# Performance work log

Measured on AMD Instinct MI355X. Metric: run time of the kernel, lower is better.

## Reference

```python
import jax, jax.numpy as jnp
import numpy as np

B, H, W, C = 16, 112, 112, 128
WS, SS, NH = 7, 3, 4  # window_size, shift_size, num_heads
EPS = 1e-5


def _ln(x, g, b):
    m = jnp.mean(x, axis=-1, keepdims=True)
    v = jnp.var(x, axis=-1, keepdims=True)
    return (x - m) * jax.lax.rsqrt(v + EPS) * g + b


def _rel_index(w):
    # standard Swin relative-position index, [w*w, w*w] int
    coords = np.stack(np.meshgrid(np.arange(w), np.arange(w), indexing='ij'))  # [2,w,w]
    flat = coords.reshape(2, -1)                      # [2, N]
    rel = (flat[:, :, None] - flat[:, None, :]).transpose(1, 2, 0)  # [N,N,2]
    rel = rel + (w - 1)
    return rel[..., 0] * (2 * w - 1) + rel[..., 1]


def _attn_mask(Hp, Wp, w, s):
    # standard Swin shifted-window attention mask, [nW, N, N] float32 (0 / -100)
    img = np.zeros((Hp, Wp))
    cnt = 0
    for hs in (slice(0, -w), slice(-w, -s), slice(-s, None)):
        for ws_ in (slice(0, -w), slice(-w, -s), slice(-s, None)):
            img[hs, ws_] = cnt
            cnt += 1
    mw = img.reshape(Hp // w, w, Wp // w, w).transpose(0, 2, 1, 3).reshape(-1, w * w)
    d = mw[:, None, :] - mw[:, :, None]
    return np.where(d != 0, -100.0, 0.0).astype(np.float32)


def setup_inputs() -> dict:
    key = jax.random.key(0)
    ks = jax.random.split(key, 8)
    f = lambda k, shape: jax.random.normal(k, shape, dtype=jnp.float32) * 0.02
    return dict(
        x=jax.random.normal(ks[0], (B, H, W, C), dtype=jnp.float32),
        norm1_g=jnp.ones((C,), jnp.float32), norm1_b=jnp.zeros((C,), jnp.float32),
        qkv_w=f(ks[1], (C, 3 * C)), qkv_b=jnp.zeros((3 * C,), jnp.float32),
        rel_table=f(ks[2], ((2 * WS - 1) ** 2, NH)),
        proj_w=f(ks[3], (C, C)), proj_b=jnp.zeros((C,), jnp.float32),
        norm2_g=jnp.ones((C,), jnp.float32), norm2_b=jnp.zeros((C,), jnp.float32),
        fc1_w=f(ks[4], (C, 4 * C)), fc1_b=jnp.zeros((4 * C,), jnp.float32),
        fc2_w=f(ks[5], (4 * C, C)), fc2_b=jnp.zeros((C,), jnp.float32),
    )


def reference(x, norm1_g, norm1_b, qkv_w, qkv_b, rel_table, proj_w, proj_b,
              norm2_g, norm2_b, fc1_w, fc1_b, fc2_w, fc2_b):
    w, s, nH = WS, SS, NH
    hd = C // nH
    N = w * w
    scale = hd ** -0.5

    shortcut = x
    xn = _ln(x, norm1_g, norm1_b)
    # cyclic shift (H, W already multiples of w -> no padding)
    xs = jnp.roll(xn, (-s, -s), axis=(1, 2)) if s > 0 else xn
    # window partition -> [B*nW, N, C]
    wins = xs.reshape(B, H // w, w, W // w, w, C).transpose(0, 1, 3, 2, 4, 5).reshape(-1, N, C)

    qkv = wins @ qkv_w + qkv_b  # [M, N, 3C]
    q, k, v = [t.reshape(-1, N, nH, hd).transpose(0, 2, 1, 3)
               for t in jnp.split(qkv, 3, axis=-1)]
    attn = jnp.einsum('mhqd,mhkd->mhqk', q * scale, k)  # [M, nH, N, N]

    idx = _rel_index(w)  # static numpy [N, N]
    bias = rel_table[idx.reshape(-1)].reshape(N, N, nH).transpose(2, 0, 1)  # [nH, N, N]
    attn = attn + bias[None]

    if s > 0:
        mask = jnp.asarray(_attn_mask(H, W, w, s))  # [nW, N, N] static
        nW = mask.shape[0]
        attn = (attn.reshape(B, nW, nH, N, N) + mask[None, :, None]).reshape(-1, nH, N, N)

    attn = jax.nn.softmax(attn, axis=-1)
    out = jnp.einsum('mhqk,mhkd->mhqd', attn, v).transpose(0, 2, 1, 3).reshape(-1, N, C)
    out = out @ proj_w + proj_b

    # window reverse + unshift
    x_attn = out.reshape(B, H // w, W // w, w, w, C).transpose(0, 1, 3, 2, 4, 5).reshape(B, H, W, C)
    if s > 0:
        x_attn = jnp.roll(x_attn, (s, s), axis=(1, 2))

    x1 = shortcut + x_attn
    xn2 = _ln(x1, norm2_g, norm2_b)
    hdd = jax.nn.gelu(xn2 @ fc1_w + fc1_b, approximate=False)  # torch nn.GELU (exact)
    return x1 + (hdd @ fc2_w + fc2_b)
```

## Files before the change

kernel.cpp:

```cpp
#include <hip/hip_runtime.h>
#include <stdint.h>

typedef unsigned short u16;
typedef unsigned int   u32;
typedef __attribute__((ext_vector_type(8))) short bh8;
typedef __attribute__((ext_vector_type(4))) float f32x4;

#define SCALE 0.17677669529663687f
#define MFMA  __builtin_amdgcn_mfma_f32_16x16x32_bf16

#define WS_QKV  0
#define WS_PROJ 49152
#define WS_F1   65536
#define WS_F2   131072
#define WS_M    196608
#define WS_QB   327680
#define WS_S1   328448
#define WS_T1   329472

__device__ __forceinline__ u16 f2bf(float f){
    u32 i; __builtin_memcpy(&i,&f,4); i += 0x7fffu + ((i>>16)&1u); return (u16)(i>>16);
}
__device__ __forceinline__ u32 cvtpk(float lo, float hi){
    u32 r; asm("v_cvt_pk_bf16_f32 %0, %1, %2" : "=v"(r) : "v"(lo), "v"(hi)); return r;
}
__device__ __forceinline__ float rcpf(float v){
    float r; asm("v_rcp_f32 %0, %1" : "=v"(r) : "v"(v)); return r;
}
__device__ __forceinline__ float gelu_f(float x){
    float ax = fabsf(x);
    float z  = ax * 0.70710678118654752f;
    float t  = rcpf(fmaf(0.3275911f, z, 1.0f));
    float p  = t * fmaf(t, fmaf(t, fmaf(t, fmaf(t, 1.061405429f, -1.453152027f),
                                        1.421413741f), -0.284496736f), 0.254829592f);
    float e  = __expf(-z * z);
    float y  = fmaf(-p, e, 1.0f);
    return fmaf(0.5f * ax, y, 0.5f * x);
}
union BH8U { bh8 v; u32 u[4]; };

__global__ void prep_k(const float* __restrict__ qkvw, const float* __restrict__ projw,
                       const float* __restrict__ f1w,  const float* __restrict__ f2w,
                       const float* __restrict__ rel,  const float* __restrict__ qkvb,
                       const float* __restrict__ n2g,  const float* __restrict__ n2b,
                       const float* __restrict__ f1b,  u16* __restrict__ ws)
{
    int idx = blockIdx.x * 256 + threadIdx.x;
    if (idx < 49152) {
        int c = idx / 384, j = idx % 384;
        float v = qkvw[idx] * (j < 128 ? SCALE : 1.0f);
        ws[WS_QKV + j * 128 + c] = f2bf(v);
    } else if (idx < 65536) {
        int i = idx - 49152; int k = i >> 7, j = i & 127;
        int pk = (k & ~31) | ((k & 15) << 1) | ((k >> 4) & 1);
        ws[WS_PROJ + j * 128 + pk] = f2bf(projw[i]);
    } else if (idx < 131072) {
        int i = idx - 65536; int c = i >> 9, j = i & 511;
        ws[WS_F1 + j * 128 + c] = f2bf(f1w[i] * n2g[c]);
    } else if (idx < 196608) {
        int i = idx - 131072; int k = i >> 7, j = i & 127;
        ws[WS_F2 + j * 512 + k] = f2bf(f2w[i]);
    } else if (idx < 262144) {
        int m = idx - 196608;
        int jr = m & 3, lane = (m >> 2) & 63, tct = (m >> 8) & 15;
        int h = (m >> 12) & 3, cls = (m >> 14) & 3;
        int rt = tct >> 2, ct = tct & 3;
        int row = rt * 16 + (lane >> 4) * 4 + jr, key = ct * 16 + (lane & 15);
        float v;
        if (row < 49 && key < 49) {
            int ri = row / 7, rc = row % 7, ki = key / 7, kc = key % 7;
            v = rel[((ri - ki + 6) * 13 + (rc - kc + 6)) * 4 + h];
            int rH = (cls & 2) ? (ri < 4 ? 1 : 2) : 0, rW = (cls & 1) ? (rc < 4 ? 1 : 2) : 0;
            int kH = (cls & 2) ? (ki < 4 ? 1 : 2) : 0, kW = (cls & 1) ? (kc < 4 ? 1 : 2) : 0;
            if (rH * 3 + rW != kH * 3 + kW) v -= 100.0f;
        } else v = -30000.0f;
        ((float*)(ws + WS_M))[m] = v;
    } else if (idx < 262528) {
        int j = idx - 262144;
        ((float*)(ws + WS_QB))[j] = qkvb[j] * (j < 128 ? SCALE : 1.0f);
    } else if (idx < 263040) {
        int j = idx - 262528;
        float s1 = 0.f, t1 = 0.f;
        for (int c = 0; c < 128; ++c) {
            float w = f1w[c * 512 + j];
            s1 = fmaf(n2g[c], w, s1);
            t1 = fmaf(n2b[c], w, t1);
        }
        ((float*)(ws + WS_S1))[j] = s1;
        ((float*)(ws + WS_T1))[j] = f1b[j] + t1;
    }
}

__global__ __launch_bounds__(256, 3) void swin_attn_k(
    const float* __restrict__ x, const float* __restrict__ n1g, const float* __restrict__ n1b,
    const float* __restrict__ projb, const u16* __restrict__ ws, float* __restrict__ out)
{
    __shared__ u16 arena[16384];
    __shared__ u16 vt[9216];
    const int tid = threadIdx.x, h = tid >> 6, lane = tid & 63;
    const int c15 = lane & 15, g = lane >> 4;
    const int m = blockIdx.x, b = m >> 8, hb = (m >> 4) & 15, wb = m & 15;
    const int cls = ((hb == 15) ? 2 : 0) | ((wb == 15) ? 1 : 0);
    const float* QB = (const float*)(ws + WS_QB);
    const float* Mb = (const float*)(ws + WS_M) + (size_t)((cls * 4 + h) * 16) * 256;

    {
        const int t = h * 16 + (lane >> 2), ss = lane & 3;
        if (t < 49) {
            const int td = (t * 37) >> 8, tm = t - td * 7;
            int hs = hb * 7 + td + 3;  if (hs >= 112) hs -= 112;
            int wsw = wb * 7 + tm + 3; if (wsw >= 112) wsw -= 112;
            const float* px = x + (size_t)((b * 112 + hs) * 112 + wsw) * 128 + ss * 32;
            float4 xv[8];
            #pragma unroll
            for (int i = 0; i < 8; ++i) xv[i] = *(const float4*)(px + i * 4);
            float s = 0.f, q = 0.f;
            #pragma unroll
            for (int i = 0; i < 8; ++i) {
                s += xv[i].x + xv[i].y + xv[i].z + xv[i].w;
                q += xv[i].x*xv[i].x + xv[i].y*xv[i].y + xv[i].z*xv[i].z + xv[i].w*xv[i].w;
            }
            s += __shfl_xor(s, 1); q += __shfl_xor(q, 1);
            s += __shfl_xor(s, 2); q += __shfl_xor(q, 2);
            float mean = s * (1.f/128.f), var = q * (1.f/128.f) - mean * mean;
            float rstd = rsqrtf(var + 1e-5f);
            const float* pg = n1g + ss * 32; const float* pb = n1b + ss * 32;
            #pragma unroll
            for (int i = 0; i < 4; ++i) {
                float4 a = xv[2*i], c = xv[2*i+1];
                float4 g1 = *(const float4*)(pg + i*8),  g2 = *(const float4*)(pg + i*8 + 4);
                float4 b1 = *(const float4*)(pb + i*8),  b2 = *(const float4*)(pb + i*8 + 4);
                uint4 w;
                w.x = cvtpk((a.x-mean)*rstd*g1.x + b1.x, (a.y-mean)*rstd*g1.y + b1.y);
                w.y = cvtpk((a.z-mean)*rstd*g1.z + b1.z, (a.w-mean)*rstd*g1.w + b1.w);
                w.z = cvtpk((c.x-mean)*rstd*g2.x + b2.x, (c.y-mean)*rstd*g2.y + b2.y);
                w.w = cvtpk((c.z-mean)*rstd*g2.z + b2.z, (c.w-mean)*rstd*g2.w + b2.w);
                *(uint4*)&arena[t * 136 + ss * 32 + i * 8] = w;
            }
        } else {
            #pragma unroll
            for (int i = 0; i < 4; ++i) *(uint4*)&arena[t * 136 + (lane & 3) * 32 + i * 8] = (uint4){0,0,0,0};
        }
    }
    __syncthreads();

    {
        bh8 avf[2][4];
        #pragma unroll
        for (int jt = 0; jt < 2; ++jt)
            #pragma unroll
            for (int kc = 0; kc < 4; ++kc)
                avf[jt][kc] = *(const bh8*)&ws[WS_QKV + (256 + h*32 + jt*16 + c15)*128 + kc*32 + g*8];
        const float vb0 = QB[256 + h*32 + c15], vb1 = QB[256 + h*32 + 16 + c15];
        #pragma unroll
        for (int tt = 0; tt < 4; ++tt) {
            bh8 xf[4];
            #pragma unroll
            for (int kc = 0; kc < 4; ++kc)
                xf[kc] = *(const bh8*)&arena[(tt*16 + c15)*136 + kc*32 + g*8];
            f32x4 D0 = {0,0,0,0}, D1 = {0,0,0,0};
            #pragma unroll
            for (int kc = 0; kc < 4; ++kc) { D0 = MFMA(xf[kc], avf[0][kc], D0, 0,0,0); D1 = MFMA(xf[kc], avf[1][kc], D1, 0,0,0); }
            uint2 p0, p1;
            p0.x = cvtpk(D0[0]+vb0, D0[1]+vb0); p0.y = cvtpk(D0[2]+vb0, D0[3]+vb0);
            p1.x = cvtpk(D1[0]+vb1, D1[1]+vb1); p1.y = cvtpk(D1[2]+vb1, D1[3]+vb1);
            *(uint2*)&vt[h*2304 + c15*72        + tt*16 + g*4] = p0;
            *(uint2*)&vt[h*2304 + (16+c15)*72   + tt*16 + g*4] = p1;
        }
    }

    bh8 qf[4], kf[4];
    {
        bh8 aqf[2][4], akf[2][4];
        #pragma unroll
        for (int jt = 0; jt < 2; ++jt)
            #pragma unroll
            for (int kc = 0; kc < 4; ++kc) {
                aqf[jt][kc] = *(const bh8*)&ws[WS_QKV + (      h*32 + jt*16 + c15)*128 + kc*32 + g*8];
                akf[jt][kc] = *(const bh8*)&ws[WS_QKV + (128 + h*32 + jt*16 + c15)*128 + kc*32 + g*8];
            }
        const float4 qb0 = *(const float4*)(QB + h*32 + g*4);
        const float4 qb1 = *(const float4*)(QB + h*32 + 16 + g*4);
        const float4 kb0 = *(const float4*)(QB + 128 + h*32 + g*4);
        const float4 kb1 = *(const float4*)(QB + 128 + h*32 + 16 + g*4);
        #pragma unroll
        for (int tt = 0; tt < 4; ++tt) {
            bh8 xf[4];
            #pragma unroll
            for (int kc = 0; kc < 4; ++kc)
                xf[kc] = *(const bh8*)&arena[(tt*16 + c15)*136 + kc*32 + g*8];
            f32x4 Dq0={0,0,0,0}, Dq1={0,0,0,0}, Dk0={0,0,0,0}, Dk1={0,0,0,0};
            #pragma unroll
            for (int kc = 0; kc < 4; ++kc) {
                Dq0 = MFMA(aqf[0][kc], xf[kc], Dq0, 0,0,0);
                Dq1 = MFMA(aqf[1][kc], xf[kc], Dq1, 0,0,0);
                Dk0 = MFMA(akf[0][kc], xf[kc], Dk0, 0,0,0);
                Dk1 = MFMA(akf[1][kc], xf[kc], Dk1, 0,0,0);
            }
            BH8U qu, ku;
            qu.u[0] = cvtpk(Dq0[0]+qb0.x, Dq0[1]+qb0.y); qu.u[1] = cvtpk(Dq0[2]+qb0.z, Dq0[3]+qb0.w);
            qu.u[2] = cvtpk(Dq1[0]+qb1.x, Dq1[1]+qb1.y); qu.u[3] = cvtpk(Dq1[2]+qb1.z, Dq1[3]+qb1.w);
            ku.u[0] = cvtpk(Dk0[0]+kb0.x, Dk0[1]+kb0.y); ku.u[1] = cvtpk(Dk0[2]+kb0.z, Dk0[3]+kb0.w);
            ku.u[2] = cvtpk(Dk1[0]+kb1.x, Dk1[1]+kb1.y); ku.u[3] = cvtpk(Dk1[2]+kb1.z, Dk1[3]+kb1.w);
            qf[tt] = qu.v; kf[tt] = ku.v;
        }
    }
    __syncthreads();

    f32x4 p[4][4]; f32x4 inv4[4];
    #pragma unroll
    for (int rt = 0; rt < 4; ++rt) {
        #pragma unroll
        for (int ct = 0; ct < 4; ++ct) {
            f32x4 macc = *(const f32x4*)(Mb + (rt*4 + ct)*256 + lane*4);
            p[rt][ct] = MFMA(qf[rt], kf[ct], macc, 0,0,0);
        }
        #pragma unroll
        for (int ct = 0; ct < 4; ++ct)
            #pragma unroll
            for (int jr = 0; jr < 4; ++jr) p[rt][ct][jr] = __expf(p[rt][ct][jr]);
        f32x4 t = p[rt][0] + p[rt][1] + p[rt][2] + p[rt][3];
        #pragma unroll
        for (int jr = 0; jr < 4; ++jr) {
            float v = t[jr];
            v += __shfl_xor(v, 1); v += __shfl_xor(v, 2);
            v += __shfl_xor(v, 4); v += __shfl_xor(v, 8);
            inv4[rt][jr] = rcpf(v + 1e-30f);
        }
    }

    char* Pbase = (char*)arena + h * 8192;
    #pragma unroll
    for (int rt = 0; rt < 4; ++rt)
        #pragma unroll
        for (int jr = 0; jr < 4; ++jr) {
            const int row = rt*16 + g*4 + jr, sw = (row & 7) << 4;
            #pragma unroll
            for (int ct = 0; ct < 4; ++ct)
                *(u16*)(Pbase + ((row*128 + (ct*16 + c15)*2) ^ sw)) = f2bf(p[rt][ct][jr]);
        }
    asm volatile("s_waitcnt lgkmcnt(0)" ::: "memory");

    f32x4 o[4][2];
    #pragma unroll
    for (int rt = 0; rt < 4; ++rt) { o[rt][0] = (f32x4){0,0,0,0}; o[rt][1] = (f32x4){0,0,0,0}; }
    {
        bh8 vf[2][2];
        #pragma unroll
        for (int ct = 0; ct < 2; ++ct)
            #pragma unroll
            for (int kc = 0; kc < 2; ++kc)
                vf[ct][kc] = *(const bh8*)&vt[h*2304 + (ct*16 + c15)*72 + kc*32 + g*8];
        #pragma unroll
        for (int rt = 0; rt < 4; ++rt) {
            const int row = rt*16 + c15, sw = (row & 7) << 4;
            #pragma unroll
            for (int kc = 0; kc < 2; ++kc) {
                bh8 pa = *(const bh8*)(Pbase + ((row*128 + kc*64 + g*16) ^ sw));
                o[rt][0] = MFMA(pa, vf[0][kc], o[rt][0], 0,0,0);
                o[rt][1] = MFMA(pa, vf[1][kc], o[rt][1], 0,0,0);
            }
        }
    }
    __syncthreads();

    #pragma unroll
    for (int rt = 0; rt < 4; ++rt)
        #pragma unroll
        for (int jr = 0; jr < 4; ++jr) {
            const int row = rt*16 + g*4 + jr;
            u32 pk_ = cvtpk(o[rt][0][jr] * inv4[rt][jr], o[rt][1][jr] * inv4[rt][jr]);
            *(u32*)&arena[row*136 + h*32 + 2*c15] = pk_;
        }
    __syncthreads();

    {
        bh8 wfp[2][4];
        #pragma unroll
        for (int ct2 = 0; ct2 < 2; ++ct2)
            #pragma unroll
            for (int kc = 0; kc < 4; ++kc)
                wfp[ct2][kc] = *(const bh8*)&ws[WS_PROJ + (h*32 + ct2*16 + c15)*128 + kc*32 + g*8];
        f32x4 pacc[4][2];
        #pragma unroll
        for (int rt = 0; rt < 4; ++rt) { pacc[rt][0] = (f32x4){0,0,0,0}; pacc[rt][1] = (f32x4){0,0,0,0}; }
        #pragma unroll
        for (int rt = 0; rt < 4; ++rt) {
            bh8 af[4];
            #pragma unroll
            for (int kc = 0; kc < 4; ++kc)
                af[kc] = *(const bh8*)&arena[(rt*16 + c15)*136 + kc*32 + g*8];
            #pragma unroll
            for (int kc = 0; kc < 4; ++kc) {
                pacc[rt][0] = MFMA(af[kc], wfp[0][kc], pacc[rt][0], 0,0,0);
                pacc[rt][1] = MFMA(af[kc], wfp[1][kc], pacc[rt][1], 0,0,0);
            }
        }
        const int col0 = h*32 + c15, col1 = col0 + 16;
        const float pb0 = projb[col0], pb1 = projb[col1];
        #pragma unroll
        for (int rt = 0; rt < 4; ++rt)
            #pragma unroll
            for (int jr = 0; jr < 4; ++jr) {
                const int t = rt*16 + g*4 + jr;
                if (t < 49) {
                    const int td = (t * 37) >> 8, tm = t - td * 7;
                    int hs = hb*7 + td + 3;  if (hs >= 112) hs -= 112;
                    int wsw = wb*7 + tm + 3; if (wsw >= 112) wsw -= 112;
                    const size_t base = (size_t)((b*112 + hs)*112 + wsw) * 128;
                    out[base + col0] = pacc[rt][0][jr] + pb0 + x[base + col0];
                    out[base + col1] = pacc[rt][1][jr] + pb1 + x[base + col1];
                }
            }
    }
}

__global__ __launch_bounds__(512, 2) void swin_mlp_k(
    float* __restrict__ xio, const float* __restrict__ f2b, const u16* __restrict__ ws)
{
    __shared__ u16 xnb[128 * 136];
    __shared__ u16 hbuf[128 * 136];
    __shared__ float2 stats[128];
    const int tid = threadIdx.x, w = tid >> 6, lane = tid & 63;
    const int c15 = lane & 15, g = lane >> 4;
    const size_t tok0 = (size_t)blockIdx.x * 128;
    const float* S1 = (const float*)(ws + WS_S1);
    const float* T1 = (const float*)(ws + WS_T1);

    {
        const int t = tid >> 2, ss = tid & 3;
        const float* px = xio + (tok0 + t) * 128 + ss * 32;
        float4 xv[8];
        #pragma unroll
        for (int i = 0; i < 8; ++i) xv[i] = *(const float4*)(px + i * 4);
        float s = 0.f, q = 0.f;
        #pragma unroll
        for (int i = 0; i < 8; ++i) {
            s += xv[i].x + xv[i].y + xv[i].z + xv[i].w;
            q += xv[i].x*xv[i].x + xv[i].y*xv[i].y + xv[i].z*xv[i].z + xv[i].w*xv[i].w;
        }
        s += __shfl_xor(s, 1); q += __shfl_xor(q, 1);
        s += __shfl_xor(s, 2); q += __shfl_xor(q, 2);
        float mean = s * (1.f/128.f), var = q * (1.f/128.f) - mean * mean;
        float rstd = rsqrtf(var + 1e-5f);
        #pragma unroll
        for (int i = 0; i < 4; ++i) {
            float4 a = xv[2*i], c = xv[2*i+1];
            uint4 wv;
            wv.x = cvtpk(a.x, a.y); wv.y = cvtpk(a.z, a.w);
            wv.z = cvtpk(c.x, c.y); wv.w = cvtpk(c.z, c.w);
            *(uint4*)&xnb[t * 136 + ss * 32 + i * 8] = wv;
        }
        if (ss == 0) stats[t] = (float2){rstd, rstd * mean};
    }
    __syncthreads();

    const int jc = w * 16 + c15;
    f32x4 acc[8];
    #pragma unroll
    for (int rt = 0; rt < 8; ++rt) acc[rt] = (f32x4){0,0,0,0};

    bh8 wf1a[4];
    #pragma unroll
    for (int kc = 0; kc < 4; ++kc)
        wf1a[kc] = *(const bh8*)&ws[WS_F1 + jc*128 + kc*32 + g*8];

    #pragma unroll
    for (int chunk = 0; chunk < 4; ++chunk) {
        bh8 wf2[4], wf1n[4];
        #pragma unroll
        for (int kc = 0; kc < 4; ++kc)
            wf2[kc] = *(const bh8*)&ws[WS_F2 + jc*512 + chunk*128 + kc*32 + g*8];
        if (chunk < 3) {
            #pragma unroll
            for (int kc = 0; kc < 4; ++kc)
                wf1n[kc] = *(const bh8*)&ws[WS_F1 + ((chunk+1)*128 + jc)*128 + kc*32 + g*8];
        }
        const float s1 = S1[chunk*128 + jc], t1 = T1[chunk*128 + jc];

        #pragma unroll
        for (int rt = 0; rt < 8; ++rt) {
            bh8 af[4];
            #pragma unroll
            for (int kc = 0; kc < 4; ++kc)
                af[kc] = *(const bh8*)&xnb[(rt*16 + c15)*136 + kc*32 + g*8];
            f32x4 D = {0,0,0,0};
            #pragma unroll
            for (int kc = 0; kc < 4; ++kc) D = MFMA(af[kc], wf1a[kc], D, 0,0,0);
            #pragma unroll
            for (int jr = 0; jr < 4; ++jr) {
                const int row = rt*16 + g*4 + jr;
                float2 st = stats[row];
                float hv = gelu_f(fmaf(st.x, D[jr], fmaf(-st.y, s1, t1)));
                hbuf[row*136 + jc] = f2bf(hv);
            }
        }
        __syncthreads();

        #pragma unroll
        for (int rt = 0; rt < 8; ++rt) {
            bh8 ha[4];
            #pragma unroll
            for (int kc = 0; kc < 4; ++kc)
                ha[kc] = *(const bh8*)&hbuf[(rt*16 + c15)*136 + kc*32 + g*8];
            #pragma unroll
            for (int kc = 0; kc < 4; ++kc)
                acc[rt] = MFMA(ha[kc], wf2[kc], acc[rt], 0,0,0);
        }
        if (chunk < 3) {
            __syncthreads();
            #pragma unroll
            for (int kc = 0; kc < 4; ++kc) wf1a[kc] = wf1n[kc];
        }
    }

    const float cb = f2b[jc];
    #pragma unroll
    for (int rt = 0; rt < 8; ++rt)
        #pragma unroll
        for (int jr = 0; jr < 4; ++jr) {
            const size_t r = (tok0 + rt*16 + g*4 + jr) * 128;
            xio[r + jc] += acc[rt][jr] + cb;
        }
}

extern "C" void kernel_launch(void* const* d_in, const int* in_sizes, int n_in,
                              void* d_out, int out_size, void* d_ws, size_t ws_size,
                              hipStream_t stream)
{
    const float* x    = (const float*)d_in[0];
    const float* n1g  = (const float*)d_in[1];
    const float* n1b  = (const float*)d_in[2];
    const float* qkvw = (const float*)d_in[3];
    const float* qkvb = (const float*)d_in[4];
    const float* rel  = (const float*)d_in[5];
    const float* pw   = (const float*)d_in[6];
    const float* pb   = (const float*)d_in[7];
    const float* n2g  = (const float*)d_in[8];
    const float* n2b  = (const float*)d_in[9];
    const float* f1w  = (const float*)d_in[10];
    const float* f1b  = (const float*)d_in[11];
    const float* f2w  = (const float*)d_in[12];
    const float* f2b  = (const float*)d_in[13];
    float* out = (float*)d_out;
    u16* ws = (u16*)d_ws;

    prep_k<<<1028, 256, 0, stream>>>(qkvw, pw, f1w, f2w, rel, qkvb, n2g, n2b, f1b, ws);
    swin_attn_k<<<4096, 256, 0, stream>>>(x, n1g, n1b, pb, ws, out);
    swin_mlp_k<<<1568, 512, 0, stream>>>(out, f2b, ws);
}
```

Measured before the change: 284.9 us.

## Restructure MLP kernel so each wave owns 32 tokens, removing block barriers

The MLP kernel now uses 256 threads, and each wave independently processes 32 tokens across all hidden columns. Token activations are held in registers, and the GELU intermediate goes to a per-wave swizzled LDS scratch, so block-wide __syncthreads and the shared LN stats are eliminated. Weights for fc1 and fc2 are streamed from global/L2 per wave rather than shared across waves via column splitting. This trades more weight traffic from cache for no inter-wave synchronization and fewer LDS bank conflicts.

```diff
diff --git a/kernel.cpp b/kernel.cpp
--- a/kernel.cpp
+++ b/kernel.cpp
@@ -315,112 +315,94 @@
     }
 }
 
-__global__ __launch_bounds__(512, 2) void swin_mlp_k(
+__global__ __launch_bounds__(256, 2) void swin_mlp_k(
     float* __restrict__ xio, const float* __restrict__ f2b, const u16* __restrict__ ws)
 {
-    __shared__ u16 xnb[128 * 136];
-    __shared__ u16 hbuf[128 * 136];
-    __shared__ float2 stats[128];
+    __shared__ char scratch[32768];
     const int tid = threadIdx.x, w = tid >> 6, lane = tid & 63;
     const int c15 = lane & 15, g = lane >> 4;
-    const size_t tok0 = (size_t)blockIdx.x * 128;
+    const size_t T0 = (size_t)blockIdx.x * 128 + w * 32;
     const float* S1 = (const float*)(ws + WS_S1);
     const float* T1 = (const float*)(ws + WS_T1);
-
-    {
-        const int t = tid >> 2, ss = tid & 3;
-        const float* px = xio + (tok0 + t) * 128 + ss * 32;
-        float4 xv[8];
-        #pragma unroll
-        for (int i = 0; i < 8; ++i) xv[i] = *(const float4*)(px + i * 4);
+    char* SB0 = scratch + w * 8192;
+    const int sw = (c15 & 7) << 4;
+
+    bh8 xB[2][4];
+    float2 st[2];
+    #pragma unroll
+    for (int rt = 0; rt < 2; ++rt) {
+        const float* px = xio + (T0 + rt*16 + c15) * 128 + g * 8;
         float s = 0.f, q = 0.f;
         #pragma unroll
-        for (int i = 0; i < 8; ++i) {
-            s += xv[i].x + xv[i].y + xv[i].z + xv[i].w;
-            q += xv[i].x*xv[i].x + xv[i].y*xv[i].y + xv[i].z*xv[i].z + xv[i].w*xv[i].w;
-        }
-        s += __shfl_xor(s, 1); q += __shfl_xor(q, 1);
-        s += __shfl_xor(s, 2); q += __shfl_xor(q, 2);
+        for (int kc = 0; kc < 4; ++kc) {
+            float4 a = *(const float4*)(px + kc*32);
+            float4 b = *(const float4*)(px + kc*32 + 4);
+            s += a.x+a.y+a.z+a.w + b.x+b.y+b.z+b.w;
+            q += a.x*a.x+a.y*a.y+a.z*a.z+a.w*a.w + b.x*b.x+b.y*b.y+b.z*b.z+b.w*b.w;
+            BH8U u;
+            u.u[0] = cvtpk(a.x, a.y); u.u[1] = cvtpk(a.z, a.w);
+            u.u[2] = cvtpk(b.x, b.y); u.u[3] = cvtpk(b.z, b.w);
+            xB[rt][kc] = u.v;
+        }
+        s += __shfl_xor(s, 16); q += __shfl_xor(q, 16);
+        s += __shfl_xor(s, 32); q += __shfl_xor(q, 32);
         float mean = s * (1.f/128.f), var = q * (1.f/128.f) - mean * mean;
         float rstd = rsqrtf(var + 1e-5f);
-        #pragma unroll
-        for (int i = 0; i < 4; ++i) {
-            float4 a = xv[2*i], c = xv[2*i+1];
-            uint4 wv;
-            wv.x = cvtpk(a.x, a.y); wv.y = cvtpk(a.z, a.w);
-            wv.z = cvtpk(c.x, c.y); wv.w = cvtpk(c.z, c.w);
-            *(uint4*)&xnb[t * 136 + ss * 32 + i * 8] = wv;
-        }
-        if (ss == 0) stats[t] = (float2){rstd, rstd * mean};
-    }
-    __syncthreads();
-
-    const int jc = w * 16 + c15;
-    f32x4 acc[8];
-    #pragma unroll
-    for (int rt = 0; rt < 8; ++rt) acc[rt] = (f32x4){0,0,0,0};
-
-    bh8 wf1a[4];
-    #pragma unroll
-    for (int kc = 0; kc < 4; ++kc)
-        wf1a[kc] = *(const bh8*)&ws[WS_F1 + jc*128 + kc*32 + g*8];
-
-    #pragma unroll
+        st[rt] = (float2){rstd, rstd * mean};
+    }
+
+    f32x4 acc[2][8];
+    #pragma unroll
+    for (int rt = 0; rt < 2; ++rt)
+        #pragma unroll
+        for (int ct = 0; ct < 8; ++ct) acc[rt][ct] = (f32x4){0,0,0,0};
+
     for (int chunk = 0; chunk < 4; ++chunk) {
-        bh8 wf2[4], wf1n[4];
-        #pragma unroll
-        for (int kc = 0; kc < 4; ++kc)
-            wf2[kc] = *(const bh8*)&ws[WS_F2 + jc*512 + chunk*128 + kc*32 + g*8];
-        if (chunk < 3) {
-            #pragma unroll
-            for (int kc = 0; kc < 4; ++kc)
-                wf1n[kc] = *(const bh8*)&ws[WS_F1 + ((chunk+1)*128 + jc)*128 + kc*32 + g*8];
-        }
-        const float s1 = S1[chunk*128 + jc], t1 = T1[chunk*128 + jc];
-
-        #pragma unroll
-        for (int rt = 0; rt < 8; ++rt) {
-            bh8 af[4];
-            #pragma unroll
-            for (int kc = 0; kc < 4; ++kc)
-                af[kc] = *(const bh8*)&xnb[(rt*16 + c15)*136 + kc*32 + g*8];
-            f32x4 D = {0,0,0,0};
-            #pragma unroll
-            for (int kc = 0; kc < 4; ++kc) D = MFMA(af[kc], wf1a[kc], D, 0,0,0);
-            #pragma unroll
-            for (int jr = 0; jr < 4; ++jr) {
-                const int row = rt*16 + g*4 + jr;
-                float2 st = stats[row];
-                float hv = gelu_f(fmaf(st.x, D[jr], fmaf(-st.y, s1, t1)));
-                hbuf[row*136 + jc] = f2bf(hv);
-            }
-        }
-        __syncthreads();
-
-        #pragma unroll
-        for (int rt = 0; rt < 8; ++rt) {
-            bh8 ha[4];
-            #pragma unroll
-            for (int kc = 0; kc < 4; ++kc)
-                ha[kc] = *(const bh8*)&hbuf[(rt*16 + c15)*136 + kc*32 + g*8];
-            #pragma unroll
-            for (int kc = 0; kc < 4; ++kc)
-                acc[rt] = MFMA(ha[kc], wf2[kc], acc[rt], 0,0,0);
-        }
-        if (chunk < 3) {
-            __syncthreads();
-            #pragma unroll
-            for (int kc = 0; kc < 4; ++kc) wf1a[kc] = wf1n[kc];
-        }
-    }
-
-    const float cb = f2b[jc];
-    #pragma unroll
-    for (int rt = 0; rt < 8; ++rt)
+        #pragma unroll
+        for (int jt = 0; jt < 8; ++jt) {
+            bh8 w1f[4];
+            #pragma unroll
+            for (int kc = 0; kc < 4; ++kc)
+                w1f[kc] = *(const bh8*)&ws[WS_F1 + (chunk*128 + jt*16 + c15)*128 + kc*32 + g*8];
+            float4 s1v = *(const float4*)(S1 + chunk*128 + jt*16 + g*4);
+            float4 t1v = *(const float4*)(T1 + chunk*128 + jt*16 + g*4);
+            #pragma unroll
+            for (int rt = 0; rt < 2; ++rt) {
+                f32x4 D = {0,0,0,0};
+                #pragma unroll
+                for (int kc = 0; kc < 4; ++kc) D = MFMA(w1f[kc], xB[rt][kc], D, 0,0,0);
+                float h0 = gelu_f(fmaf(st[rt].x, D[0], fmaf(-st[rt].y, s1v.x, t1v.x)));
+                float h1 = gelu_f(fmaf(st[rt].x, D[1], fmaf(-st[rt].y, s1v.y, t1v.y)));
+                float h2 = gelu_f(fmaf(st[rt].x, D[2], fmaf(-st[rt].y, s1v.z, t1v.z)));
+                float h3 = gelu_f(fmaf(st[rt].x, D[3], fmaf(-st[rt].y, s1v.w, t1v.w)));
+                uint2 hp; hp.x = cvtpk(h0, h1); hp.y = cvtpk(h2, h3);
+                *(uint2*)(SB0 + rt*4096 + ((c15*256 + jt*32 + g*8) ^ sw)) = hp;
+            }
+        }
+        #pragma unroll
+        for (int kt = 0; kt < 4; ++kt) {
+            bh8 hA0 = *(const bh8*)(SB0        + ((c15*256 + kt*64 + g*16) ^ sw));
+            bh8 hA1 = *(const bh8*)(SB0 + 4096 + ((c15*256 + kt*64 + g*16) ^ sw));
+            #pragma unroll
+            for (int ct = 0; ct < 8; ++ct) {
+                bh8 w2f = *(const bh8*)&ws[WS_F2 + (ct*16 + c15)*512 + chunk*128 + kt*32 + g*8];
+                acc[0][ct] = MFMA(hA0, w2f, acc[0][ct], 0, 0, 0);
+                acc[1][ct] = MFMA(hA1, w2f, acc[1][ct], 0, 0, 0);
+            }
+        }
+    }
+
+    float f2bv[8];
+    #pragma unroll
+    for (int ct = 0; ct < 8; ++ct) f2bv[ct] = f2b[ct*16 + c15];
+    #pragma unroll
+    for (int rt = 0; rt < 2; ++rt)
         #pragma unroll
         for (int jr = 0; jr < 4; ++jr) {
-            const size_t r = (tok0 + rt*16 + g*4 + jr) * 128;
-            xio[r + jc] += acc[rt][jr] + cb;
+            float* pr = xio + (T0 + rt*16 + g*4 + jr) * 128 + c15;
+            #pragma unroll
+            for (int ct = 0; ct < 8; ++ct)
+                pr[ct*16] += acc[rt][ct][jr] + f2bv[ct];
         }
 }
 
@@ -447,5 +429,5 @@
 
     prep_k<<<1028, 256, 0, stream>>>(qkvw, pw, f1w, f2w, rel, qkvb, n2g, n2b, f1b, ws);
     swin_attn_k<<<4096, 256, 0, stream>>>(x, n1g, n1b, pb, ws, out);
-    swin_mlp_k<<<1568, 512, 0, stream>>>(out, f2b, ws);
-}
+    swin_mlp_k<<<1568, 256, 0, stream>>>(out, f2b, ws);
+}
```

Result: slower. 385.1 us (+35.1%).
